# Optimization experiments

Hardware: AMD Instinct MI355X
Metric: run time of the kernel (lower is better)

## Reference

```python
import jax, jax.numpy as jnp
import numpy as np

B, L, D_IN, D_OUT, K = 2, 4096, 256, 256, 16


def setup_inputs() -> dict:
    key = jax.random.key(0)
    k_u, k_ev, k_ew, k_m = jax.random.split(key, 4)
    u = jax.random.normal(k_u, (B, L, D_IN), dtype=jnp.float32)
    eigenvectors = jax.random.normal(k_ev, (K, L), dtype=jnp.float32)
    # original takes loaded eigenvalues ** 0.25; emulate positive spectrum then 0.25 power
    eigenvalues = jax.random.uniform(k_ew, (K,), dtype=jnp.float32, minval=1e-3, maxval=1.0) ** 0.25
    # xavier_uniform_ for M of shape (k, d_in, d_out): bound = sqrt(6/(d_in+d_out))
    bound = float(np.sqrt(6.0 / (D_IN + D_OUT)))
    M = jax.random.uniform(k_m, (K, D_IN, D_OUT), dtype=jnp.float32, minval=-bound, maxval=bound)
    return {"u": u, "eigenvectors": eigenvectors, "eigenvalues": eigenvalues, "M": M}


def reference(u, eigenvectors, eigenvalues, M):
    # u: (B, L, D); eigenvectors: (k, L); eigenvalues: (k,); M: (k, D_in, D_out)
    Lseq = u.shape[1]
    ev_fft = jnp.fft.rfft(eigenvectors, axis=-1)          # (k, F) complex
    u_fft = jnp.fft.rfft(jnp.swapaxes(u, 1, 2), axis=-1)  # (B, D, F)
    p_fft = u_fft[:, None, :, :] * ev_fft[None, :, None, :]  # (B, k, D, F)
    conv = jnp.fft.irfft(p_fft, n=Lseq, axis=-1)          # (B, k, D, L)
    return jnp.einsum('bkdl,k,kdp->blp', conv, eigenvalues, M)
```

## Files before the change

### kernel.cpp

```cpp
#include <hip/hip_runtime.h>


typedef unsigned int uint;
using u16x8 = __attribute__((ext_vector_type(8))) unsigned short;
using s16x8 = __attribute__((ext_vector_type(8))) short;
using f32x4 = __attribute__((ext_vector_type(4))) float;

__device__ __forceinline__ unsigned short f2bf(float f) {
  uint u = __float_as_uint(f);
  uint r = (u + 0x7FFF + ((u >> 16) & 1)) >> 16;
  return (unsigned short)r;
}
__device__ __forceinline__ float bf2f(unsigned short h) {
  return __uint_as_float(((uint)h) << 16);
}

template <int NT>
__device__ __forceinline__ void fft4096(float2* __restrict__ a,
                                        float2* __restrict__ b,
                                        const float2* __restrict__ tw, int tid) {
  float2* src = a;
  float2* dst = b;
#pragma unroll
  for (int s = 0; s < 12; s += 2) {
    const int m = 1 << s;
#pragma unroll
    for (int it = 0; it < 1024 / NT; ++it) {
      int idx = tid + it * NT;
      int i   = idx & (m - 1);
      int jm  = idx - i;
      float2 A0 = src[idx];
      float2 B0 = src[idx + 1024];
      float2 C0 = src[idx + 2048];
      float2 D0 = src[idx + 3072];
      float2 w1 = tw[jm];
      float2 w2 = make_float2(w1.x * w1.x - w1.y * w1.y, 2.f * w1.x * w1.y);
      float2 w3 = make_float2(w2.x * w1.x - w2.y * w1.y, w2.x * w1.y + w2.y * w1.x);
      float acx = A0.x + C0.x, acy = A0.y + C0.y;
      float amx = A0.x - C0.x, amy = A0.y - C0.y;
      float bdx = B0.x + D0.x, bdy = B0.y + D0.y;
      float bmx = B0.x - D0.x, bmy = B0.y - D0.y;
      float2 y0 = make_float2(acx + bdx, acy + bdy);
      float2 t2 = make_float2(acx - bdx, acy - bdy);
      float2 t1 = make_float2(amx + bmy, amy - bmx);
      float2 t3 = make_float2(amx - bmy, amy + bmx);
      int base = idx + 3 * jm;
      dst[base]         = y0;
      dst[base + m]     = make_float2(w1.x * t1.x - w1.y * t1.y, w1.x * t1.y + w1.y * t1.x);
      dst[base + 2 * m] = make_float2(w2.x * t2.x - w2.y * t2.y, w2.x * t2.y + w2.y * t2.x);
      dst[base + 3 * m] = make_float2(w3.x * t3.x - w3.y * t3.y, w3.x * t3.y + w3.y * t3.x);
    }
    __syncthreads();
    float2* t = src; src = dst; dst = t;
  }
}

template <int NT>
__device__ __forceinline__ void build_tw(float2* tw, int tid) {
  for (int t = tid; t < 1024; t += NT) {
    float ang = -(float)t * (6.283185307179586f / 4096.0f);
    float s, c;
    sincosf(ang, &s, &c);
    tw[t] = make_float2(c, s);
  }
}

__global__ __launch_bounds__(256) void prep(const float* __restrict__ M,
                                            const float* __restrict__ u,
                                            unsigned short* __restrict__ Mt,
                                            unsigned short* __restrict__ ubT) {
  __shared__ float t[64][65];
  const int bid = blockIdx.x;
  const int r = threadIdx.x >> 2, c0 = (threadIdx.x & 3) * 16;

  const float* src;
  unsigned short* dst;
  size_t src_stride;
  if (bid < 256) {
    const int k = bid >> 4, d0 = ((bid >> 2) & 3) * 64, p0 = (bid & 3) * 64;
    src = M + ((size_t)k * 256 + d0) * 256 + p0;
    dst = Mt + ((size_t)k * 256 + p0 + r) * 256 + d0 + c0;
    src_stride = 256;
  } else {
    const int b2 = bid - 256;
    const int l0 = (b2 & 63) * 64, d0 = ((b2 >> 6) & 3) * 64, plane = b2 >> 8;
    src = u + ((size_t)plane * 4096 + l0) * 256 + d0;
    dst = ubT + ((size_t)plane * 256 + d0 + r) * 4096 + l0 + c0;
    src_stride = 256;
  }
#pragma unroll
  for (int j = 0; j < 4; ++j) {
    float4 v = *(const float4*)(src + (size_t)r * src_stride + c0 + j * 4);
    t[r][c0 + j * 4 + 0] = v.x;
    t[r][c0 + j * 4 + 1] = v.y;
    t[r][c0 + j * 4 + 2] = v.z;
    t[r][c0 + j * 4 + 3] = v.w;
  }
  __syncthreads();
  u16x8 o0, o1;
#pragma unroll
  for (int j = 0; j < 8; ++j) o0[j] = f2bf(t[c0 + j][r]);
#pragma unroll
  for (int j = 0; j < 8; ++j) o1[j] = f2bf(t[c0 + 8 + j][r]);
  *(u16x8*)dst = o0;
  *(u16x8*)(dst + 8) = o1;
}

__global__ __launch_bounds__(1024) void fft_fwd(const unsigned short* __restrict__ ubT,
                                                const float* __restrict__ ev,
                                                const float* __restrict__ lam,
                                                unsigned short* __restrict__ Ut,
                                                float* __restrict__ Hbuf) {
  __shared__ float2 A[4096];
  __shared__ float2 Bb[4096];
  __shared__ float2 tw[1024];
  const int tid = threadIdx.x;
  const int bid = blockIdx.x;
  build_tw<1024>(tw, tid);

  if (bid < 256) {
    const int plane = bid >> 7;
    const int jj = bid & 127;
    const int pair = (jj & 7) * 16 + (jj >> 3);
    const int d0 = pair * 2;
    const unsigned short* r0 = ubT + ((size_t)plane * 256 + d0) * 4096;
    const unsigned short* r1 = r0 + 4096;
    const int l0 = tid * 4;
    ushort4 a4 = *(const ushort4*)(r0 + l0);
    ushort4 b4 = *(const ushort4*)(r1 + l0);
    A[l0 + 0] = make_float2(bf2f(a4.x), bf2f(b4.x));
    A[l0 + 1] = make_float2(bf2f(a4.y), bf2f(b4.y));
    A[l0 + 2] = make_float2(bf2f(a4.z), bf2f(b4.z));
    A[l0 + 3] = make_float2(bf2f(a4.w), bf2f(b4.w));
    __syncthreads();
    fft4096<1024>(A, Bb, tw, tid);
    unsigned short* Up = Ut + (size_t)plane * 4096 * 256 + d0;
#pragma unroll
    for (int i = 0; i < 2; ++i) {
      int f = tid + i * 1024;
      float u0x, u0y, u1x, u1y;
      if (f == 0) {
        float2 X0 = A[0], Xn = A[2048];
        u0x = X0.x; u1x = X0.y;
        u0y = Xn.x; u1y = Xn.y;
      } else {
        float2 Xa = A[f], Xb = A[4096 - f];
        u0x = 0.5f * (Xa.x + Xb.x);
        u0y = 0.5f * (Xa.y - Xb.y);
        u1x = 0.5f * (Xa.y + Xb.y);
        u1y = 0.5f * (Xb.x - Xa.x);
      }
      ushort2 re = make_ushort2(f2bf(u0x), f2bf(u1x));
      ushort2 im = make_ushort2(f2bf(u0y), f2bf(u1y));
      *(ushort2*)(Up + (size_t)f * 256)          = re;
      *(ushort2*)(Up + (size_t)(2048 + f) * 256) = im;
    }
  } else {
    const int k = bid - 256;
    const float* eb = ev + (size_t)k * 4096;
#pragma unroll
    for (int i = 0; i < 4; ++i) {
      int l = tid + i * 1024;
      A[l] = make_float2(eb[l], 0.0f);
    }
    __syncthreads();
    fft4096<1024>(A, Bb, tw, tid);
    const float sc = lam[k] * (1.0f / 4096.0f);
    float* Hp = Hbuf + (size_t)k * 4096;
#pragma unroll
    for (int i = 0; i < 2; ++i) {
      int f = tid + i * 1024;
      float2 X = A[f];
      Hp[f] = sc * X.x;
      Hp[2048 + f] = (f == 0) ? sc * A[2048].x : sc * X.y;
    }
  }
}

__global__ __launch_bounds__(512) void gemm_spec(const unsigned short* __restrict__ Ut,
                                                 const unsigned short* __restrict__ Mt,
                                                 const float* __restrict__ Hbuf,
                                                 float* __restrict__ Chat) {
  __shared__ unsigned short Ms[2][64 * 256];
  __shared__ float Hlds[16 * 128];
  const int gi  = blockIdx.x;
  const int xcd = gi & 7;
  const int gj  = gi >> 3;
  const int fb    = (xcd * 4 + (gj & 3)) * 64;
  const int p0    = ((gj >> 2) & 3) * 64;
  const int plane = gj >> 4;

  const int tid  = threadIdx.x;
  const int lane = tid & 63;
  const int wave = tid >> 6;
  const int half = wave >> 2;
  const int w4   = wave & 3;
  const int th   = tid & 255;

#pragma unroll
  for (int it = 0; it < 4; ++it) {
    int i2 = tid + it * 512;
    int k = i2 >> 7, rem = i2 & 127;
    Hlds[i2] = Hbuf[(size_t)k * 4096 + (rem >> 6) * 2048 + fb + (rem & 63)];
  }

  const unsigned short* Up = Ut + (size_t)plane * 4096 * 256;
  const int binoff = w4 * 16 + (lane & 15);
  const int bin = fb + binoff;
  const int dly = (lane >> 4) * 8;
  s16x8 ure[8], uim[8];
#pragma unroll
  for (int kk = 0; kk < 8; ++kk) {
    ure[kk] = *(const s16x8*)(Up + (size_t)(fb + binoff) * 256 + kk * 32 + dly);
    uim[kk] = *(const s16x8*)(Up + (size_t)(2048 + fb + binoff) * 256 + kk * 32 + dly);
  }

  const unsigned short* Mbase = Mt + (size_t)half * 8 * 65536;
  u16x8 mreg[8];
#pragma unroll
  for (int it = 0; it < 8; ++it) {
    int cl = th + it * 256;
    int r = cl >> 5, c = cl & 31;
    mreg[it] = *(const u16x8*)(Mbase + (size_t)(p0 + r) * 256 + c * 8);
  }

  f32x4 cre[4], cim[4];
#pragma unroll
  for (int m = 0; m < 4; ++m) {
    cre[m] = (f32x4){0.f, 0.f, 0.f, 0.f};
    cim[m] = (f32x4){0.f, 0.f, 0.f, 0.f};
  }

  for (int kh = 0; kh < 8; ++kh) {
    if (kh > 0) __syncthreads();
#pragma unroll
    for (int it = 0; it < 8; ++it) {
      int cl = th + it * 256;
      int r = cl >> 5, c = cl & 31;
      *(u16x8*)(&Ms[half][r * 256 + ((c ^ (r & 7)) * 8)]) = mreg[it];
    }
    if (kh < 7) {
      const unsigned short* Mk = Mbase + (size_t)(kh + 1) * 65536;
#pragma unroll
      for (int it = 0; it < 8; ++it) {
        int cl = th + it * 256;
        int r = cl >> 5, c = cl & 31;
        mreg[it] = *(const u16x8*)(Mk + (size_t)(p0 + r) * 256 + c * 8);
      }
    }
    __syncthreads();

    f32x4 are[4], aim[4];
#pragma unroll
    for (int m = 0; m < 4; ++m) {
      are[m] = (f32x4){0.f, 0.f, 0.f, 0.f};
      aim[m] = (f32x4){0.f, 0.f, 0.f, 0.f};
    }
#pragma unroll
    for (int kk = 0; kk < 8; ++kk) {
      const int kc = kk * 4 + (lane >> 4);
#pragma unroll
      for (int m = 0; m < 4; ++m) {
        int row = m * 16 + (lane & 15);
        s16x8 af = *(const s16x8*)(&Ms[half][row * 256 + ((kc ^ (row & 7)) * 8)]);
        are[m] = __builtin_amdgcn_mfma_f32_16x16x32_bf16(af, ure[kk], are[m], 0, 0, 0);
        aim[m] = __builtin_amdgcn_mfma_f32_16x16x32_bf16(af, uim[kk], aim[m], 0, 0, 0);
      }
    }
    const int k = kh + 8 * half;
    float hre = Hlds[k * 128 + binoff];
    float hs  = Hlds[k * 128 + 64 + binoff];
    bool sp = (bin == 0);
    float him = sp ? 0.0f : hs;
    float hA  = sp ? hs : hre;
#pragma unroll
    for (int m = 0; m < 4; ++m)
#pragma unroll
      for (int i = 0; i < 4; ++i) {
        cre[m][i] += hre * are[m][i] - him * aim[m][i];
        cim[m][i] += hA * aim[m][i] + him * are[m][i];
      }
  }

  __syncthreads();
  float* Red = (float*)Ms;
#pragma unroll
  for (int m = 0; m < 4; ++m)
#pragma unroll
    for (int i = 0; i < 4; ++i) {
      Red[(m * 4 + i) * 512 + tid]        = cre[m][i];
      Red[(16 + m * 4 + i) * 512 + tid]   = cim[m][i];
    }
  __syncthreads();
  if (tid < 256) {
#pragma unroll
    for (int m = 0; m < 4; ++m)
#pragma unroll
      for (int i = 0; i < 4; ++i) {
        cre[m][i] += Red[(m * 4 + i) * 512 + tid + 256];
        cim[m][i] += Red[(16 + m * 4 + i) * 512 + tid + 256];
      }
    float* Cp = Chat + ((size_t)plane * 256 + p0) * 4096;
#pragma unroll
    for (int m = 0; m < 4; ++m)
#pragma unroll
      for (int i = 0; i < 4; ++i) {
        int pl = m * 16 + (lane >> 4) * 4 + i;
        Cp[(size_t)pl * 4096 + bin]        = cre[m][i];
        Cp[(size_t)pl * 4096 + 2048 + bin] = cim[m][i];
      }
  }
}

__global__ __launch_bounds__(1024) void ifft_store(const float* __restrict__ Chat,
                                                   float* __restrict__ ytmp) {
  __shared__ float2 A[4096];
  __shared__ float2 Bb[4096];
  __shared__ float2 tw[1024];
  const int tid = threadIdx.x;
  const int p0 = blockIdx.x * 2;
  const int plane = blockIdx.y;
  const float* C0 = Chat + ((size_t)plane * 256 + p0) * 4096;
  const float* C1 = C0 + 4096;
  build_tw<1024>(tw, tid);

  if (tid == 0) {
    A[0]    = make_float2(C0[0], -C1[0]);
    A[2048] = make_float2(C0[2048], -C1[2048]);
  } else {
    int f = tid;
    float cr0 = C0[f], ci0 = C0[2048 + f];
    float cr1 = C1[f], ci1 = C1[2048 + f];
    A[f]        = make_float2(cr0 - ci1, -(ci0 + cr1));
    A[4096 - f] = make_float2(cr0 + ci1, ci0 - cr1);
  }
  {
    int f = tid + 1024;
    float cr0 = C0[f], ci0 = C0[2048 + f];
    float cr1 = C1[f], ci1 = C1[2048 + f];
    A[f]        = make_float2(cr0 - ci1, -(ci0 + cr1));
    A[4096 - f] = make_float2(cr0 + ci1, ci0 - cr1);
  }
  __syncthreads();
  fft4096<1024>(A, Bb, tw, tid);

  float* y0 = ytmp + ((size_t)plane * 256 + p0) * 4096;
  float* y1 = y0 + 4096;
#pragma unroll
  for (int i = 0; i < 4; ++i) {
    int l = tid + i * 1024;
    float2 g = A[l];
    y0[l] = g.x;
    y1[l] = -g.y;
  }
}

__global__ __launch_bounds__(256) void tr_out(const float* __restrict__ ytmp,
                                              float* __restrict__ out) {
  __shared__ float t[64][65];
  const int l0 = blockIdx.x * 64, p0 = blockIdx.y * 64, plane = blockIdx.z;
  const int r = threadIdx.x >> 2, c0 = (threadIdx.x & 3) * 16;
  const float* src = ytmp + ((size_t)plane * 256 + p0 + r) * 4096 + l0;
#pragma unroll
  for (int j = 0; j < 4; ++j) {
    float4 v = *(const float4*)(src + c0 + j * 4);
    t[r][c0 + j * 4 + 0] = v.x;
    t[r][c0 + j * 4 + 1] = v.y;
    t[r][c0 + j * 4 + 2] = v.z;
    t[r][c0 + j * 4 + 3] = v.w;
  }
  __syncthreads();
  float* dst = out + ((size_t)plane * 4096 + l0 + r) * 256 + p0 + c0;
#pragma unroll
  for (int q = 0; q < 4; ++q) {
    float4 o;
    o.x = t[c0 + q * 4 + 0][r];
    o.y = t[c0 + q * 4 + 1][r];
    o.z = t[c0 + q * 4 + 2][r];
    o.w = t[c0 + q * 4 + 3][r];
    *(float4*)(dst + q * 4) = o;
  }
}

extern "C" void kernel_launch(void* const* d_in, const int* in_sizes, int n_in,
                              void* d_out, int out_size, void* d_ws,
                              size_t ws_size, hipStream_t stream) {
  const float* u   = (const float*)d_in[0];
  const float* ev  = (const float*)d_in[1];
  const float* lam = (const float*)d_in[2];
  const float* M   = (const float*)d_in[3];
  float* out = (float*)d_out;

  char* ws = (char*)d_ws;
  float* Hbuf         = (float*)ws;
  unsigned short* Mt  = (unsigned short*)(ws + (256 << 10));
  unsigned short* ubT = (unsigned short*)(ws + (256 << 10) + (2 << 20));
  unsigned short* Ut  = (unsigned short*)(ws + (256 << 10) + (6 << 20));
  float* Chat         = (float*)(ws + (256 << 10) + (10 << 20));
  float* ytmp         = (float*)(ws + (256 << 10) + (18 << 20));

  prep<<<768, 256, 0, stream>>>(M, u, Mt, ubT);
  fft_fwd<<<272, 1024, 0, stream>>>(ubT, ev, lam, Ut, Hbuf);
  gemm_spec<<<256, 512, 0, stream>>>(Ut, Mt, Hbuf, Chat);
  ifft_store<<<dim3(128, 2), 1024, 0, stream>>>(Chat, ytmp);
  tr_out<<<dim3(64, 4, 2), 256, 0, stream>>>(ytmp, out);
}
```

Before: 117.2 us.

## Move eigenvector FFT into prep, async-load M tiles via LDS DMA in spectral GEMM

The eigenvector FFTs (two per block via a real-pair trick) move into the prep kernel, which now uses 1024-thread blocks each handling four transpose tiles. fft_fwd then only transforms the input signal. The spectral GEMM now double-buffers M tiles through global_load_lds direct-to-LDS copies instead of register staging. Its waves are re-split across d halves and bin groups with a 4-way reduction at the end, aiming to overlap loads with MFMA and cut register pressure. The cost is more LDS (double buffer), an extra reduction pass, and a sync per k step.

```diff
diff --git a/kernel.cpp b/kernel.cpp
--- a/kernel.cpp
+++ b/kernel.cpp
@@ -13,6 +13,12 @@
 }
 __device__ __forceinline__ float bf2f(unsigned short h) {
   return __uint_as_float(((uint)h) << 16);
+}
+
+__device__ __forceinline__ void gload_lds16(const void* g, void* l) {
+  __builtin_amdgcn_global_load_lds(
+      (const __attribute__((address_space(1))) unsigned int*)g,
+      (__attribute__((address_space(3))) unsigned int*)l, 16, 0, 0);
 }
 
 template <int NT>
@@ -65,52 +71,93 @@
   }
 }
 
-__global__ __launch_bounds__(256) void prep(const float* __restrict__ M,
-                                            const float* __restrict__ u,
-                                            unsigned short* __restrict__ Mt,
-                                            unsigned short* __restrict__ ubT) {
-  __shared__ float t[64][65];
+__global__ __launch_bounds__(1024) void prep(const float* __restrict__ M,
+                                             const float* __restrict__ u,
+                                             const float* __restrict__ ev,
+                                             const float* __restrict__ lam,
+                                             unsigned short* __restrict__ Mt,
+                                             unsigned short* __restrict__ ubT,
+                                             float* __restrict__ Hbuf) {
+  __shared__ float smem[18432];
   const int bid = blockIdx.x;
-  const int r = threadIdx.x >> 2, c0 = (threadIdx.x & 3) * 16;
-
-  const float* src;
-  unsigned short* dst;
-  size_t src_stride;
-  if (bid < 256) {
-    const int k = bid >> 4, d0 = ((bid >> 2) & 3) * 64, p0 = (bid & 3) * 64;
-    src = M + ((size_t)k * 256 + d0) * 256 + p0;
-    dst = Mt + ((size_t)k * 256 + p0 + r) * 256 + d0 + c0;
-    src_stride = 256;
+  const int tid = threadIdx.x;
+
+  if (bid < 192) {
+    const int sub  = tid >> 8;
+    const int t256 = tid & 255;
+    const int tile = bid * 4 + sub;
+    float (*t)[65] = (float(*)[65])(smem + sub * 4160);
+    const int r = t256 >> 2, c0 = (t256 & 3) * 16;
+    const float* src;
+    unsigned short* dst;
+    if (tile < 256) {
+      const int k = tile >> 4, d0 = ((tile >> 2) & 3) * 64, pp = (tile & 3) * 64;
+      src = M + ((size_t)k * 256 + d0) * 256 + pp;
+      dst = Mt + ((size_t)k * 256 + pp + r) * 256 + d0 + c0;
+    } else {
+      const int b2 = tile - 256;
+      const int l0 = (b2 & 63) * 64, d0 = ((b2 >> 6) & 3) * 64, plane = b2 >> 8;
+      src = u + ((size_t)plane * 4096 + l0) * 256 + d0;
+      dst = ubT + ((size_t)plane * 256 + d0 + r) * 4096 + l0 + c0;
+    }
+#pragma unroll
+    for (int j = 0; j < 4; ++j) {
+      float4 v = *(const float4*)(src + (size_t)r * 256 + c0 + j * 4);
+      t[r][c0 + j * 4 + 0] = v.x;
+      t[r][c0 + j * 4 + 1] = v.y;
+      t[r][c0 + j * 4 + 2] = v.z;
+      t[r][c0 + j * 4 + 3] = v.w;
+    }
+    __syncthreads();
+    u16x8 o0, o1;
+#pragma unroll
+    for (int j = 0; j < 8; ++j) o0[j] = f2bf(t[c0 + j][r]);
+#pragma unroll
+    for (int j = 0; j < 8; ++j) o1[j] = f2bf(t[c0 + 8 + j][r]);
+    *(u16x8*)dst = o0;
+    *(u16x8*)(dst + 8) = o1;
   } else {
-    const int b2 = bid - 256;
-    const int l0 = (b2 & 63) * 64, d0 = ((b2 >> 6) & 3) * 64, plane = b2 >> 8;
-    src = u + ((size_t)plane * 4096 + l0) * 256 + d0;
-    dst = ubT + ((size_t)plane * 256 + d0 + r) * 4096 + l0 + c0;
-    src_stride = 256;
-  }
-#pragma unroll
-  for (int j = 0; j < 4; ++j) {
-    float4 v = *(const float4*)(src + (size_t)r * src_stride + c0 + j * 4);
-    t[r][c0 + j * 4 + 0] = v.x;
-    t[r][c0 + j * 4 + 1] = v.y;
-    t[r][c0 + j * 4 + 2] = v.z;
-    t[r][c0 + j * 4 + 3] = v.w;
-  }
-  __syncthreads();
-  u16x8 o0, o1;
-#pragma unroll
-  for (int j = 0; j < 8; ++j) o0[j] = f2bf(t[c0 + j][r]);
-#pragma unroll
-  for (int j = 0; j < 8; ++j) o1[j] = f2bf(t[c0 + 8 + j][r]);
-  *(u16x8*)dst = o0;
-  *(u16x8*)(dst + 8) = o1;
+    float2* A  = (float2*)smem;
+    float2* Bb = (float2*)(smem + 8192);
+    float2* tw = (float2*)(smem + 16384);
+    build_tw<1024>(tw, tid);
+    const int k0 = (bid - 192) * 2;
+    const float* e0 = ev + (size_t)k0 * 4096;
+    const float* e1 = e0 + 4096;
+#pragma unroll
+    for (int i = 0; i < 4; ++i) {
+      int l = tid + i * 1024;
+      A[l] = make_float2(e0[l], e1[l]);
+    }
+    __syncthreads();
+    fft4096<1024>(A, Bb, tw, tid);
+    const float s0 = lam[k0] * (1.0f / 4096.0f);
+    const float s1 = lam[k0 + 1] * (1.0f / 4096.0f);
+    float* H0 = Hbuf + (size_t)k0 * 4096;
+    float* H1 = H0 + 4096;
+#pragma unroll
+    for (int i = 0; i < 2; ++i) {
+      int f = tid + i * 1024;
+      float e0x, e0y, e1x, e1y;
+      if (f == 0) {
+        float2 X0 = A[0], Xn = A[2048];
+        e0x = X0.x; e1x = X0.y;
+        e0y = Xn.x; e1y = Xn.y;
+      } else {
+        float2 Xa = A[f], Xb = A[4096 - f];
+        e0x = 0.5f * (Xa.x + Xb.x);
+        e0y = 0.5f * (Xa.y - Xb.y);
+        e1x = 0.5f * (Xa.y + Xb.y);
+        e1y = 0.5f * (Xb.x - Xa.x);
+      }
+      H0[f] = s0 * e0x; H0[2048 + f] = s0 * e0y;
+      H1[f] = s1 * e1x; H1[2048 + f] = s1 * e1y;
+    }
+  }
 }
 
 __global__ __launch_bounds__(1024) void fft_fwd(const unsigned short* __restrict__ ubT,
-                                                const float* __restrict__ ev,
-                                                const float* __restrict__ lam,
-                                                unsigned short* __restrict__ Ut,
-                                                float* __restrict__ Hbuf) {
+                                                unsigned short* __restrict__ Ut) {
   __shared__ float2 A[4096];
   __shared__ float2 Bb[4096];
   __shared__ float2 tw[1024];
@@ -118,62 +165,41 @@
   const int bid = blockIdx.x;
   build_tw<1024>(tw, tid);
 
-  if (bid < 256) {
-    const int plane = bid >> 7;
-    const int jj = bid & 127;
-    const int pair = (jj & 7) * 16 + (jj >> 3);
-    const int d0 = pair * 2;
-    const unsigned short* r0 = ubT + ((size_t)plane * 256 + d0) * 4096;
-    const unsigned short* r1 = r0 + 4096;
-    const int l0 = tid * 4;
-    ushort4 a4 = *(const ushort4*)(r0 + l0);
-    ushort4 b4 = *(const ushort4*)(r1 + l0);
-    A[l0 + 0] = make_float2(bf2f(a4.x), bf2f(b4.x));
-    A[l0 + 1] = make_float2(bf2f(a4.y), bf2f(b4.y));
-    A[l0 + 2] = make_float2(bf2f(a4.z), bf2f(b4.z));
-    A[l0 + 3] = make_float2(bf2f(a4.w), bf2f(b4.w));
-    __syncthreads();
-    fft4096<1024>(A, Bb, tw, tid);
-    unsigned short* Up = Ut + (size_t)plane * 4096 * 256 + d0;
-#pragma unroll
-    for (int i = 0; i < 2; ++i) {
-      int f = tid + i * 1024;
-      float u0x, u0y, u1x, u1y;
-      if (f == 0) {
-        float2 X0 = A[0], Xn = A[2048];
-        u0x = X0.x; u1x = X0.y;
-        u0y = Xn.x; u1y = Xn.y;
-      } else {
-        float2 Xa = A[f], Xb = A[4096 - f];
-        u0x = 0.5f * (Xa.x + Xb.x);
-        u0y = 0.5f * (Xa.y - Xb.y);
-        u1x = 0.5f * (Xa.y + Xb.y);
-        u1y = 0.5f * (Xb.x - Xa.x);
-      }
-      ushort2 re = make_ushort2(f2bf(u0x), f2bf(u1x));
-      ushort2 im = make_ushort2(f2bf(u0y), f2bf(u1y));
-      *(ushort2*)(Up + (size_t)f * 256)          = re;
-      *(ushort2*)(Up + (size_t)(2048 + f) * 256) = im;
-    }
-  } else {
-    const int k = bid - 256;
-    const float* eb = ev + (size_t)k * 4096;
-#pragma unroll
-    for (int i = 0; i < 4; ++i) {
-      int l = tid + i * 1024;
-      A[l] = make_float2(eb[l], 0.0f);
-    }
-    __syncthreads();
-    fft4096<1024>(A, Bb, tw, tid);
-    const float sc = lam[k] * (1.0f / 4096.0f);
-    float* Hp = Hbuf + (size_t)k * 4096;
-#pragma unroll
-    for (int i = 0; i < 2; ++i) {
-      int f = tid + i * 1024;
-      float2 X = A[f];
-      Hp[f] = sc * X.x;
-      Hp[2048 + f] = (f == 0) ? sc * A[2048].x : sc * X.y;
-    }
+  const int plane = bid >> 7;
+  const int jj = bid & 127;
+  const int pair = (jj & 7) * 16 + (jj >> 3);
+  const int d0 = pair * 2;
+  const unsigned short* r0 = ubT + ((size_t)plane * 256 + d0) * 4096;
+  const unsigned short* r1 = r0 + 4096;
+  const int l0 = tid * 4;
+  ushort4 a4 = *(const ushort4*)(r0 + l0);
+  ushort4 b4 = *(const ushort4*)(r1 + l0);
+  A[l0 + 0] = make_float2(bf2f(a4.x), bf2f(b4.x));
+  A[l0 + 1] = make_float2(bf2f(a4.y), bf2f(b4.y));
+  A[l0 + 2] = make_float2(bf2f(a4.z), bf2f(b4.z));
+  A[l0 + 3] = make_float2(bf2f(a4.w), bf2f(b4.w));
+  __syncthreads();
+  fft4096<1024>(A, Bb, tw, tid);
+  unsigned short* Up = Ut + (size_t)plane * 4096 * 256 + d0;
+#pragma unroll
+  for (int i = 0; i < 2; ++i) {
+    int f = tid + i * 1024;
+    float u0x, u0y, u1x, u1y;
+    if (f == 0) {
+      float2 X0 = A[0], Xn = A[2048];
+      u0x = X0.x; u1x = X0.y;
+      u0y = Xn.x; u1y = Xn.y;
+    } else {
+      float2 Xa = A[f], Xb = A[4096 - f];
+      u0x = 0.5f * (Xa.x + Xb.x);
+      u0y = 0.5f * (Xa.y - Xb.y);
+      u1x = 0.5f * (Xa.y + Xb.y);
+      u1y = 0.5f * (Xb.x - Xa.x);
+    }
+    ushort2 re = make_ushort2(f2bf(u0x), f2bf(u1x));
+    ushort2 im = make_ushort2(f2bf(u0y), f2bf(u1y));
+    *(ushort2*)(Up + (size_t)f * 256)          = re;
+    *(ushort2*)(Up + (size_t)(2048 + f) * 256) = im;
   }
 }
 
@@ -181,7 +207,7 @@
                                                  const unsigned short* __restrict__ Mt,
                                                  const float* __restrict__ Hbuf,
                                                  float* __restrict__ Chat) {
-  __shared__ unsigned short Ms[2][64 * 256];
+  __shared__ unsigned short Ms[2][2][64 * 256];
   __shared__ float Hlds[16 * 128];
   const int gi  = blockIdx.x;
   const int xcd = gi & 7;
@@ -194,8 +220,9 @@
   const int lane = tid & 63;
   const int wave = tid >> 6;
   const int half = wave >> 2;
+  const int dh   = (wave >> 1) & 1;
+  const int bg   = wave & 1;
   const int w4   = wave & 3;
-  const int th   = tid & 255;
 
 #pragma unroll
   for (int it = 0; it < 4; ++it) {
@@ -205,109 +232,140 @@
   }
 
   const unsigned short* Up = Ut + (size_t)plane * 4096 * 256;
-  const int binoff = w4 * 16 + (lane & 15);
-  const int bin = fb + binoff;
   const int dly = (lane >> 4) * 8;
-  s16x8 ure[8], uim[8];
-#pragma unroll
-  for (int kk = 0; kk < 8; ++kk) {
-    ure[kk] = *(const s16x8*)(Up + (size_t)(fb + binoff) * 256 + kk * 32 + dly);
-    uim[kk] = *(const s16x8*)(Up + (size_t)(2048 + fb + binoff) * 256 + kk * 32 + dly);
-  }
-
-  const unsigned short* Mbase = Mt + (size_t)half * 8 * 65536;
-  u16x8 mreg[8];
-#pragma unroll
-  for (int it = 0; it < 8; ++it) {
-    int cl = th + it * 256;
-    int r = cl >> 5, c = cl & 31;
-    mreg[it] = *(const u16x8*)(Mbase + (size_t)(p0 + r) * 256 + c * 8);
-  }
-
-  f32x4 cre[4], cim[4];
-#pragma unroll
-  for (int m = 0; m < 4; ++m) {
-    cre[m] = (f32x4){0.f, 0.f, 0.f, 0.f};
-    cim[m] = (f32x4){0.f, 0.f, 0.f, 0.f};
-  }
-
+  s16x8 ure[2][4], uim[2][4];
+#pragma unroll
+  for (int bf = 0; bf < 2; ++bf) {
+    int row = fb + bg * 32 + bf * 16 + (lane & 15);
+#pragma unroll
+    for (int kk = 0; kk < 4; ++kk) {
+      int dcol = dh * 128 + kk * 32 + dly;
+      ure[bf][kk] = *(const s16x8*)(Up + (size_t)row * 256 + dcol);
+      uim[bf][kk] = *(const s16x8*)(Up + (size_t)(2048 + row) * 256 + dcol);
+    }
+  }
+
+  int srcoff[8];
+#pragma unroll
+  for (int c = 0; c < 8; ++c) {
+    int b = w4 * 8192 + c * 1024 + lane * 16;
+    int row = b >> 9, slot = (b >> 4) & 31;
+    int slot2 = (slot & ~7) | ((slot ^ (row & 7)) & 7);
+    srcoff[c] = row * 512 + slot2 * 16;
+  }
+  const char* Mhalf = (const char*)Mt + (size_t)(half * 8) * 131072 + (size_t)p0 * 512;
+
+  f32x4 cre[4][2], cim[4][2];
+#pragma unroll
+  for (int m = 0; m < 4; ++m)
+#pragma unroll
+    for (int bf = 0; bf < 2; ++bf) {
+      cre[m][bf] = (f32x4){0.f, 0.f, 0.f, 0.f};
+      cim[m][bf] = (f32x4){0.f, 0.f, 0.f, 0.f};
+    }
+
+  {
+    const char* src = Mhalf;
+#pragma unroll
+    for (int c = 0; c < 8; ++c)
+      gload_lds16(src + srcoff[c], &Ms[0][half][w4 * 4096 + c * 512]);
+  }
+  __syncthreads();
+
+  int cur = 0;
   for (int kh = 0; kh < 8; ++kh) {
-    if (kh > 0) __syncthreads();
-#pragma unroll
-    for (int it = 0; it < 8; ++it) {
-      int cl = th + it * 256;
-      int r = cl >> 5, c = cl & 31;
-      *(u16x8*)(&Ms[half][r * 256 + ((c ^ (r & 7)) * 8)]) = mreg[it];
-    }
     if (kh < 7) {
-      const unsigned short* Mk = Mbase + (size_t)(kh + 1) * 65536;
-#pragma unroll
-      for (int it = 0; it < 8; ++it) {
-        int cl = th + it * 256;
-        int r = cl >> 5, c = cl & 31;
-        mreg[it] = *(const u16x8*)(Mk + (size_t)(p0 + r) * 256 + c * 8);
+      const char* src = Mhalf + (size_t)(kh + 1) * 131072;
+#pragma unroll
+      for (int c = 0; c < 8; ++c)
+        gload_lds16(src + srcoff[c], &Ms[cur ^ 1][half][w4 * 4096 + c * 512]);
+    }
+
+    f32x4 are[4][2], aim[4][2];
+#pragma unroll
+    for (int m = 0; m < 4; ++m)
+#pragma unroll
+      for (int bf = 0; bf < 2; ++bf) {
+        are[m][bf] = (f32x4){0.f, 0.f, 0.f, 0.f};
+        aim[m][bf] = (f32x4){0.f, 0.f, 0.f, 0.f};
       }
-    }
-    __syncthreads();
-
-    f32x4 are[4], aim[4];
-#pragma unroll
-    for (int m = 0; m < 4; ++m) {
-      are[m] = (f32x4){0.f, 0.f, 0.f, 0.f};
-      aim[m] = (f32x4){0.f, 0.f, 0.f, 0.f};
-    }
-#pragma unroll
-    for (int kk = 0; kk < 8; ++kk) {
-      const int kc = kk * 4 + (lane >> 4);
+#pragma unroll
+    for (int kk = 0; kk < 4; ++kk) {
+      const int kc = dh * 16 + kk * 4 + (lane >> 4);
 #pragma unroll
       for (int m = 0; m < 4; ++m) {
         int row = m * 16 + (lane & 15);
-        s16x8 af = *(const s16x8*)(&Ms[half][row * 256 + ((kc ^ (row & 7)) * 8)]);
-        are[m] = __builtin_amdgcn_mfma_f32_16x16x32_bf16(af, ure[kk], are[m], 0, 0, 0);
-        aim[m] = __builtin_amdgcn_mfma_f32_16x16x32_bf16(af, uim[kk], aim[m], 0, 0, 0);
+        s16x8 af = *(const s16x8*)(&Ms[cur][half][row * 256 + ((kc ^ (row & 7)) * 8)]);
+        are[m][0] = __builtin_amdgcn_mfma_f32_16x16x32_bf16(af, ure[0][kk], are[m][0], 0, 0, 0);
+        aim[m][0] = __builtin_amdgcn_mfma_f32_16x16x32_bf16(af, uim[0][kk], aim[m][0], 0, 0, 0);
+        are[m][1] = __builtin_amdgcn_mfma_f32_16x16x32_bf16(af, ure[1][kk], are[m][1], 0, 0, 0);
+        aim[m][1] = __builtin_amdgcn_mfma_f32_16x16x32_bf16(af, uim[1][kk], aim[m][1], 0, 0, 0);
       }
     }
     const int k = kh + 8 * half;
-    float hre = Hlds[k * 128 + binoff];
-    float hs  = Hlds[k * 128 + 64 + binoff];
-    bool sp = (bin == 0);
-    float him = sp ? 0.0f : hs;
-    float hA  = sp ? hs : hre;
+#pragma unroll
+    for (int bf = 0; bf < 2; ++bf) {
+      int boff = bg * 32 + bf * 16 + (lane & 15);
+      float hre = Hlds[k * 128 + boff];
+      float hs  = Hlds[k * 128 + 64 + boff];
+      bool sp = (fb + boff == 0);
+      float him = sp ? 0.0f : hs;
+      float hA  = sp ? hs : hre;
+#pragma unroll
+      for (int m = 0; m < 4; ++m)
+#pragma unroll
+        for (int i = 0; i < 4; ++i) {
+          cre[m][bf][i] += hre * are[m][bf][i] - him * aim[m][bf][i];
+          cim[m][bf][i] += hA * aim[m][bf][i] + him * are[m][bf][i];
+        }
+    }
+    __syncthreads();
+    cur ^= 1;
+  }
+
+  float* Red = (float*)Ms;
+#pragma unroll
+  for (int m = 0; m < 4; ++m)
+#pragma unroll
+    for (int bf = 0; bf < 2; ++bf)
+#pragma unroll
+      for (int i = 0; i < 4; ++i)
+        Red[((m * 2 + bf) * 4 + i) * 512 + tid] = cre[m][bf][i];
+  __syncthreads();
+  float rsum[32];
+  if (tid < 128) {
+#pragma unroll
+    for (int s = 0; s < 32; ++s)
+      rsum[s] = Red[s * 512 + tid] + Red[s * 512 + tid + 128] +
+                Red[s * 512 + tid + 256] + Red[s * 512 + tid + 384];
+  }
+  __syncthreads();
+#pragma unroll
+  for (int m = 0; m < 4; ++m)
+#pragma unroll
+    for (int bf = 0; bf < 2; ++bf)
+#pragma unroll
+      for (int i = 0; i < 4; ++i)
+        Red[((m * 2 + bf) * 4 + i) * 512 + tid] = cim[m][bf][i];
+  __syncthreads();
+  if (tid < 128) {
+    const int ln  = tid & 63;
+    const int bgs = tid >> 6;
+    float* Cp = Chat + ((size_t)plane * 256 + p0) * 4096;
 #pragma unroll
     for (int m = 0; m < 4; ++m)
 #pragma unroll
-      for (int i = 0; i < 4; ++i) {
-        cre[m][i] += hre * are[m][i] - him * aim[m][i];
-        cim[m][i] += hA * aim[m][i] + him * are[m][i];
-      }
-  }
-
-  __syncthreads();
-  float* Red = (float*)Ms;
-#pragma unroll
-  for (int m = 0; m < 4; ++m)
-#pragma unroll
-    for (int i = 0; i < 4; ++i) {
-      Red[(m * 4 + i) * 512 + tid]        = cre[m][i];
-      Red[(16 + m * 4 + i) * 512 + tid]   = cim[m][i];
-    }
-  __syncthreads();
-  if (tid < 256) {
-#pragma unroll
-    for (int m = 0; m < 4; ++m)
-#pragma unroll
-      for (int i = 0; i < 4; ++i) {
-        cre[m][i] += Red[(m * 4 + i) * 512 + tid + 256];
-        cim[m][i] += Red[(16 + m * 4 + i) * 512 + tid + 256];
-      }
-    float* Cp = Chat + ((size_t)plane * 256 + p0) * 4096;
-#pragma unroll
-    for (int m = 0; m < 4; ++m)
-#pragma unroll
-      for (int i = 0; i < 4; ++i) {
-        int pl = m * 16 + (lane >> 4) * 4 + i;
-        Cp[(size_t)pl * 4096 + bin]        = cre[m][i];
-        Cp[(size_t)pl * 4096 + 2048 + bin] = cim[m][i];
+      for (int bf = 0; bf < 2; ++bf) {
+        int bin = fb + bgs * 32 + bf * 16 + (ln & 15);
+#pragma unroll
+        for (int i = 0; i < 4; ++i) {
+          int s = (m * 2 + bf) * 4 + i;
+          int pl = m * 16 + (ln >> 4) * 4 + i;
+          float isum = Red[s * 512 + tid] + Red[s * 512 + tid + 128] +
+                       Red[s * 512 + tid + 256] + Red[s * 512 + tid + 384];
+          Cp[(size_t)pl * 4096 + bin]        = rsum[s];
+          Cp[(size_t)pl * 4096 + 2048 + bin] = isum;
+        }
       }
   }
 }
@@ -399,8 +457,8 @@
   float* Chat         = (float*)(ws + (256 << 10) + (10 << 20));
   float* ytmp         = (float*)(ws + (256 << 10) + (18 << 20));
 
-  prep<<<768, 256, 0, stream>>>(M, u, Mt, ubT);
-  fft_fwd<<<272, 1024, 0, stream>>>(ubT, ev, lam, Ut, Hbuf);
+  prep<<<200, 1024, 0, stream>>>(M, u, ev, lam, Mt, ubT, Hbuf);
+  fft_fwd<<<256, 1024, 0, stream>>>(ubT, Ut);
   gemm_spec<<<256, 512, 0, stream>>>(Ut, Mt, Hbuf, Chat);
   ifft_store<<<dim3(128, 2), 1024, 0, stream>>>(Chat, ytmp);
   tr_out<<<dim3(64, 4, 2), 256, 0, stream>>>(ytmp, out);
```

After: 125.3 us. 6.9% more time.
